# Kernel tuning notes

Hardware: AMD Instinct MI355X
Metric: run time of the kernel (lower is better)

Reference implementation:

```python
import jax, jax.numpy as jnp
import numpy as np

V, E, H, EH, IH = 32000, 512, 512, 512, 512
B, S, T = 32, 128, 64
COPY_COEFF = 1.0
BOS = 0

def setup_inputs() -> dict:
    key = jax.random.key(0)
    ks = jax.random.split(key, 12)
    n = jax.random.normal
    return {
        "trg_tokens": jax.random.randint(ks[0], (B, T), 0, V),
        "init_hidden": n(ks[1], (B, IH), jnp.float32),
        "enc_hs": n(ks[2], (S, B, EH), jnp.float32),
        "enc_idxs": jax.random.randint(ks[3], (B, S), 0, V),
        "emb": n(ks[4], (V, E), jnp.float32) * 0.02,
        "W_ih": n(ks[5], (4 * H, E), jnp.float32) * 0.04,
        "W_hh": n(ks[6], (4 * H, H), jnp.float32) * 0.04,
        "b_ih": jnp.zeros((4 * H,), jnp.float32),
        "b_hh": jnp.zeros((4 * H,), jnp.float32),
        "bridge_W": n(ks[7], (H, IH), jnp.float32) * 0.04,
        "bridge_b": jnp.zeros((H,), jnp.float32),
        "out_W": n(ks[8], (V, H), jnp.float32) * 0.04,
        "out_b": jnp.zeros((V,), jnp.float32),
        "copy_W": n(ks[9], (H, EH), jnp.float32) * 0.04,
        "copy_b": jnp.zeros((H,), jnp.float32),
    }


def _decode(trg_tokens, enc_idxs, init_hidden, enc_hs, emb, W_ih, W_hh, b_ih, b_hh,
            bridge_W, bridge_b, out_W, out_b, copy_W, copy_b):
    vocab = emb.shape[0]
    # bridge: tanh(Linear(init_hidden_size, hidden)), shared for h0 and c0
    h0 = jnp.tanh(init_hidden @ bridge_W.T + bridge_b)  # [B, H]
    c0 = h0
    # teacher-forced input tokens: [BOS, trg[0], ..., trg[T-2]]
    bos = jnp.full((trg_tokens.shape[0], 1), BOS, trg_tokens.dtype)
    tok_in = jnp.concatenate([bos, trg_tokens[:, :-1]], axis=1)  # [B, T]
    # copy features are step-invariant: tanh(copy_weights(enc_hs.transpose(0,1)))
    u_feat = jnp.tanh(jnp.einsum('sbe,he->bsh', enc_hs, copy_W) + copy_b)  # [B, S, H]

    def scatter_copy(s, idx):
        # replaces one-hot [S, V] bmm with a scatter-add: sum exp-scores per vocab id
        return jnp.zeros((vocab,), s.dtype).at[idx].add(s)

    def step(carry, tok):
        h, c = carry
        x = emb[tok]  # [B, E]
        gates = x @ W_ih.T + b_ih + h @ W_hh.T + b_hh  # [B, 4H], torch order i,f,g,o
        i, f, g, o = jnp.split(gates, 4, axis=-1)
        c = jax.nn.sigmoid(f) * c + jax.nn.sigmoid(i) * jnp.tanh(g)
        h = jax.nn.sigmoid(o) * jnp.tanh(c)
        score_gen = h @ out_W.T + out_b  # [B, V]
        u = jnp.einsum('bsh,bh->bs', u_feat, h)  # copy scores over source positions
        umax = jnp.max(u, axis=1, keepdims=True)
        ue = jnp.exp(u - umax)
        u_copy = jnp.log(jax.vmap(scatter_copy)(ue, enc_idxs) + 1e-35) + umax  # [B, V]
        scores = jax.nn.softmax(jnp.concatenate([score_gen, u_copy], axis=1), axis=1)
        proba = scores[:, :vocab] + COPY_COEFF * scores[:, vocab:]
        return (h, c), jnp.log(proba)

    (_, _), logp = jax.lax.scan(step, (h0, c0), tok_in.T)  # logp: [T, B, V]
    return logp


def reference(trg_tokens, init_hidden, enc_hs, enc_idxs, emb, W_ih, W_hh, b_ih, b_hh,
              bridge_W, bridge_b, out_W, out_b, copy_W, copy_b):
    return _decode(trg_tokens, enc_idxs, init_hidden, enc_hs, emb, W_ih, W_hh, b_ih, b_hh,
                   bridge_W, bridge_b, out_W, out_b, copy_W, copy_b)
```

## Files before the change

kernel.cpp:

```cpp
#include <hip/hip_runtime.h>
#include <stdint.h>

#define VOCAB 32000
#define HID   512
#define NBAT  32
#define NSRC  128
#define NTGT  64

typedef __attribute__((ext_vector_type(8))) __bf16 bf16x8;
typedef __attribute__((ext_vector_type(4))) float  f32x4;

__device__ __forceinline__ ushort f2bf(float f) {
  union { float f; uint32_t u; } v; v.f = f;
  uint32_t u = v.u;
  u += 0x7fffu + ((u >> 16) & 1u);
  return (ushort)(u >> 16);
}

__device__ __forceinline__ float sigmoidf_(float x) { return 1.0f / (1.0f + expf(-x)); }

__device__ __forceinline__ int swz(int row, int chunk16) {
  return (chunk16 * 16) ^ ((row & 7) * 16);
}

__device__ __forceinline__ f32x4 mfma16(bf16x8 a, bf16x8 b, f32x4 c) {
  return __builtin_amdgcn_mfma_f32_16x16x32_bf16(a, b, c, 0, 0, 0);
}

__global__ void init_kernel(const int* __restrict__ trg, int* __restrict__ tok_in,
                            const float* __restrict__ b_ih, const float* __restrict__ b_hh,
                            float* __restrict__ bsum, int* __restrict__ flags) {
  int i = blockIdx.x * 256 + threadIdx.x;
  if (i < 2048) {
    int t = i >> 5, b = i & 31;
    tok_in[i] = (t == 0) ? 0 : trg[b * NTGT + (t - 1)];
    bsum[i] = b_ih[i] + b_hh[i];
  }
  if (i < 1024) flags[i] = 0;
}

__global__ void cvt_kernel(const float* __restrict__ src, ushort* __restrict__ dst, int n4) {
  int i = blockIdx.x * 256 + threadIdx.x;
  if (i < n4) {
    float4 v = reinterpret_cast<const float4*>(src)[i];
    ushort4 o;
    o.x = f2bf(v.x); o.y = f2bf(v.y); o.z = f2bf(v.z); o.w = f2bf(v.w);
    reinterpret_cast<ushort4*>(dst)[i] = o;
  }
}

__global__ __launch_bounds__(256, 2)
void bridge_kernel(const float* __restrict__ init_hidden, const float* __restrict__ bW,
                   const float* __restrict__ bb, float* __restrict__ hbuf_f32,
                   ushort* __restrict__ hbuf_bf) {
  __shared__ float ih[512];
  int b = blockIdx.x, tid = threadIdx.x;
  ih[tid] = init_hidden[b * 512 + tid];
  ih[tid + 256] = init_hidden[b * 512 + 256 + tid];
  __syncthreads();
  for (int rep = 0; rep < 2; ++rep) {
    int j = tid + rep * 256;
    const float4* wr = reinterpret_cast<const float4*>(bW + (size_t)j * 512);
    float s = 0.0f;
    #pragma unroll 4
    for (int k = 0; k < 128; ++k) {
      float4 wv = wr[k];
      s += wv.x * ih[k*4] + wv.y * ih[k*4+1] + wv.z * ih[k*4+2] + wv.w * ih[k*4+3];
    }
    float v = tanhf(s + bb[j]);
    hbuf_f32[b * 512 + j] = v;
    hbuf_bf[b * 512 + j]  = f2bf(v);
  }
}

template<int AMODE, int TANH, int STATS>
__global__ __launch_bounds__(256, 2)
void gemm_bt(const void* __restrict__ Av, const ushort* __restrict__ Bw,
             const float* __restrict__ bias, float* __restrict__ C,
             const int* __restrict__ gidx, float2* __restrict__ partials,
             int N, int K, int PNB) {
  __shared__ __align__(16) char smem[32768];
  __shared__ float pm[128][2], ps[128][2];
  char* smA = smem;
  char* smB = smem + 16384;
  const int tid = threadIdx.x;
  const int w = tid >> 6, l = tid & 63;
  const int mb0 = blockIdx.x * 128, nb0 = blockIdx.y * 128;
  const int msub = (w & 1) * 64, nsub = (w >> 1) * 64;

  f32x4 acc[4][4] = {};
  const int kiters = K >> 6;
  for (int ki = 0; ki < kiters; ++ki) {
    __syncthreads();
    if (AMODE == 2) {
      const ushort* A16 = (const ushort*)Av;
      #pragma unroll
      for (int c = 0; c < 4; ++c) {
        int id = tid + c * 256;
        int row = id >> 3, kc = id & 7;
        uint4 av = *reinterpret_cast<const uint4*>(A16 + (size_t)(mb0 + row) * K + ki * 64 + kc * 8);
        int byte = row * 128 + swz(row, kc);
        *reinterpret_cast<uint4*>(smA + byte) = av;
      }
    } else {
      const float* A32 = (const float*)Av;
      #pragma unroll
      for (int c = 0; c < 8; ++c) {
        int id = tid + c * 256;
        int row = id >> 4, f4 = id & 15;
        int arow = (AMODE == 1) ? gidx[mb0 + row] : (mb0 + row);
        float4 av = *reinterpret_cast<const float4*>(A32 + (size_t)arow * K + ki * 64 + f4 * 4);
        uint32_t lo = (uint32_t)f2bf(av.x) | ((uint32_t)f2bf(av.y) << 16);
        uint32_t hi = (uint32_t)f2bf(av.z) | ((uint32_t)f2bf(av.w) << 16);
        int byte = row * 128 + swz(row, f4 >> 1) + (f4 & 1) * 8;
        *reinterpret_cast<uint2*>(smA + byte) = make_uint2(lo, hi);
      }
    }
    #pragma unroll
    for (int c = 0; c < 4; ++c) {
      int id = tid + c * 256;
      int row = id >> 3, kc = id & 7;
      uint4 bv = *reinterpret_cast<const uint4*>(Bw + (size_t)(nb0 + row) * K + ki * 64 + kc * 8);
      int byte = row * 128 + swz(row, kc);
      *reinterpret_cast<uint4*>(smB + byte) = bv;
    }
    __syncthreads();
    #pragma unroll
    for (int ks = 0; ks < 2; ++ks) {
      bf16x8 af[4], bfr[4];
      #pragma unroll
      for (int i = 0; i < 4; ++i) {
        int row = msub + i * 16 + (l & 15);
        af[i] = *reinterpret_cast<const bf16x8*>(smA + row * 128 + swz(row, ks * 4 + (l >> 4)));
      }
      #pragma unroll
      for (int i = 0; i < 4; ++i) {
        int row = nsub + i * 16 + (l & 15);
        bfr[i] = *reinterpret_cast<const bf16x8*>(smB + row * 128 + swz(row, ks * 4 + (l >> 4)));
      }
      #pragma unroll
      for (int mi = 0; mi < 4; ++mi)
        #pragma unroll
        for (int ni = 0; ni < 4; ++ni)
          acc[mi][ni] = mfma16(af[mi], bfr[ni], acc[mi][ni]);
    }
  }
  float bcol[4];
  #pragma unroll
  for (int ni = 0; ni < 4; ++ni)
    bcol[ni] = bias ? bias[nb0 + nsub + ni * 16 + (l & 15)] : 0.0f;
  #pragma unroll
  for (int mi = 0; mi < 4; ++mi) {
    #pragma unroll
    for (int ni = 0; ni < 4; ++ni) {
      int col = nb0 + nsub + ni * 16 + (l & 15);
      #pragma unroll
      for (int j = 0; j < 4; ++j) {
        int row = mb0 + msub + mi * 16 + (l >> 4) * 4 + j;
        float v = acc[mi][ni][j] + bcol[ni];
        acc[mi][ni][j] = v;
        if (TANH) v = tanhf(v);
        C[(size_t)row * N + col] = v;
      }
    }
  }
  if (STATS) {
    #pragma unroll
    for (int mi = 0; mi < 4; ++mi) {
      #pragma unroll
      for (int j = 0; j < 4; ++j) {
        float mx = fmaxf(fmaxf(acc[mi][0][j], acc[mi][1][j]), fmaxf(acc[mi][2][j], acc[mi][3][j]));
        #pragma unroll
        for (int d = 1; d < 16; d <<= 1) mx = fmaxf(mx, __shfl_xor(mx, d));
        float sx = expf(acc[mi][0][j] - mx) + expf(acc[mi][1][j] - mx)
                 + expf(acc[mi][2][j] - mx) + expf(acc[mi][3][j] - mx);
        #pragma unroll
        for (int d = 1; d < 16; d <<= 1) sx += __shfl_xor(sx, d);
        if ((l & 15) == 0) {
          int r = msub + mi * 16 + (l >> 4) * 4 + j;
          pm[r][w >> 1] = mx;
          ps[r][w >> 1] = sx;
        }
      }
    }
    __syncthreads();
    if (tid < 128) {
      float ma = pm[tid][0], mb = pm[tid][1];
      float m = fmaxf(ma, mb);
      float s = ps[tid][0] * expf(ma - m) + ps[tid][1] * expf(mb - m);
      partials[(size_t)(mb0 + tid) * PNB + blockIdx.y] = make_float2(m, s);
    }
  }
}

__global__ __launch_bounds__(256, 1)
void lstm_rec(const ushort* __restrict__ Whh_bf, const float* __restrict__ gates_x,
              float* __restrict__ hbuf_f32, ushort* __restrict__ hbuf_bf,
              int* __restrict__ flags) {
  __shared__ __align__(16) char h_lds[32 * 1024];
  __shared__ float gt[32 * 64];
  __shared__ float c_state[512];
  const int tid = threadIdx.x, w = tid >> 6, l = tid & 63;
  const int blk = blockIdx.x;
  const int gate0 = (w >> 1) * 2;
  const int mtile = (w & 1);

  bf16x8 wf[2][16];
  #pragma unroll
  for (int nt = 0; nt < 2; ++nt) {
    int grow = (gate0 + nt) * 512 + blk * 16 + (l & 15);
    const ushort* base = Whh_bf + (size_t)grow * 512 + (l >> 4) * 8;
    #pragma unroll
    for (int ks = 0; ks < 16; ++ks)
      wf[nt][ks] = *reinterpret_cast<const bf16x8*>(base + ks * 32);
  }

  for (int idx = tid; idx < 512; idx += 256) {
    int b = idx >> 4, cc = idx & 15;
    c_state[idx] = hbuf_f32[b * 512 + blk * 16 + cc];
  }

  float gpre[2][4];
  #pragma unroll
  for (int nt = 0; nt < 2; ++nt)
    #pragma unroll
    for (int j = 0; j < 4; ++j) {
      int b = mtile * 16 + (l >> 4) * 4 + j;
      gpre[nt][j] = gates_x[(size_t)b * 2048 + (gate0 + nt) * 512 + blk * 16 + (l & 15)];
    }

  for (int t = 0; t < NTGT; ++t) {
    const ushort* hsrc = hbuf_bf + (size_t)t * (32 * 512);
    #pragma unroll
    for (int c = 0; c < 8; ++c) {
      int id = tid + c * 256;
      int row = id >> 6, ch = id & 63;
      uint4 v = *reinterpret_cast<const uint4*>(hsrc + row * 512 + ch * 8);
      *reinterpret_cast<uint4*>(h_lds + row * 1024 + ((ch * 16) ^ ((row & 7) * 16))) = v;
    }
    __syncthreads();

    f32x4 acc[2];
    #pragma unroll
    for (int nt = 0; nt < 2; ++nt)
      #pragma unroll
      for (int j = 0; j < 4; ++j)
        acc[nt][j] = gpre[nt][j];
    #pragma unroll
    for (int ks = 0; ks < 16; ++ks) {
      int row = mtile * 16 + (l & 15);
      bf16x8 af = *reinterpret_cast<const bf16x8*>(
          h_lds + row * 1024 + (((ks * 4 + (l >> 4)) * 16) ^ ((row & 7) * 16)));
      acc[0] = mfma16(af, wf[0][ks], acc[0]);
      acc[1] = mfma16(af, wf[1][ks], acc[1]);
    }
    #pragma unroll
    for (int nt = 0; nt < 2; ++nt)
      #pragma unroll
      for (int j = 0; j < 4; ++j) {
        int b = mtile * 16 + (l >> 4) * 4 + j;
        gt[b * 64 + (gate0 + nt) * 16 + (l & 15)] = acc[nt][j];
      }
    __syncthreads();

    #pragma unroll
    for (int rep = 0; rep < 2; ++rep) {
      int idx = tid + rep * 256;
      int b = idx >> 4, cc = idx & 15;
      float gi = gt[b * 64 + cc],      gf = gt[b * 64 + 16 + cc];
      float gg = gt[b * 64 + 32 + cc], go = gt[b * 64 + 48 + cc];
      float cn = sigmoidf_(gf) * c_state[idx] + sigmoidf_(gi) * tanhf(gg);
      float hn = sigmoidf_(go) * tanhf(cn);
      c_state[idx] = cn;
      size_t o = (size_t)(t + 1) * (32 * 512) + b * 512 + blk * 16 + cc;
      hbuf_f32[o] = hn;
      __hip_atomic_store(&hbuf_bf[o], f2bf(hn), __ATOMIC_RELAXED, __HIP_MEMORY_SCOPE_AGENT);
    }
    asm volatile("s_waitcnt vmcnt(0)" ::: "memory");
    __syncthreads();
    if (tid == 0)
      __hip_atomic_store(&flags[blk * 32], t + 1, __ATOMIC_RELAXED, __HIP_MEMORY_SCOPE_AGENT);

    if (t + 1 < NTGT) {
      #pragma unroll
      for (int nt = 0; nt < 2; ++nt)
        #pragma unroll
        for (int j = 0; j < 4; ++j) {
          int b = mtile * 16 + (l >> 4) * 4 + j;
          gpre[nt][j] = gates_x[(size_t)((t + 1) * 32 + b) * 2048 + (gate0 + nt) * 512 + blk * 16 + (l & 15)];
        }
      if (w == 0) {
        int target = t + 1;
        while (true) {
          int f = (l < 32) ? __hip_atomic_load(&flags[l * 32], __ATOMIC_RELAXED, __HIP_MEMORY_SCOPE_AGENT)
                           : target;
          if (__all(f >= target)) break;
          __builtin_amdgcn_s_sleep(1);
        }
        __builtin_amdgcn_fence(__ATOMIC_ACQUIRE, "agent");
      }
      __syncthreads();
    }
  }
}

__global__ __launch_bounds__(256, 2)
void stats_kernel(const float2* __restrict__ partials, const float* __restrict__ hbuf_f32,
                  const float* __restrict__ u_feat, float* __restrict__ ue_out,
                  float4* __restrict__ stats) {
  __shared__ float red[256];
  __shared__ float hl[512];
  __shared__ float up[256];
  int r = blockIdx.x, tid = threadIdx.x;
  int t = r >> 5, b = r & 31;
  float m_i = -3.0e38f, s_i = 0.0f;
  if (tid < 250) { float2 p = partials[(size_t)r * 250 + tid]; m_i = p.x; s_i = p.y; }
  red[tid] = m_i; __syncthreads();
  for (int s = 128; s > 0; s >>= 1) { if (tid < s) red[tid] = fmaxf(red[tid], red[tid + s]); __syncthreads(); }
  float G = red[0]; __syncthreads();
  red[tid] = (tid < 250) ? s_i * expf(m_i - G) : 0.0f; __syncthreads();
  for (int s = 128; s > 0; s >>= 1) { if (tid < s) red[tid] += red[tid + s]; __syncthreads(); }
  float Sg = red[0]; __syncthreads();

  const float* hrow = hbuf_f32 + (size_t)(t + 1) * (32 * 512) + b * 512;
  hl[tid] = hrow[tid]; hl[tid + 256] = hrow[tid + 256];
  __syncthreads();
  {
    int s = tid & 127, half = tid >> 7;
    const float4* uf = reinterpret_cast<const float4*>(u_feat + (size_t)(s * 32 + b) * 512 + half * 256);
    const float* hh = hl + half * 256;
    float p = 0.0f;
    #pragma unroll 4
    for (int k = 0; k < 64; ++k) {
      float4 v = uf[k];
      p += v.x * hh[k*4] + v.y * hh[k*4+1] + v.z * hh[k*4+2] + v.w * hh[k*4+3];
    }
    up[tid] = p;
  }
  __syncthreads();
  float u = 0.0f;
  if (tid < 128) u = up[tid] + up[tid + 128];
  red[tid] = (tid < 128) ? u : -3.0e38f;
  __syncthreads();
  for (int s = 128; s > 0; s >>= 1) { if (tid < s) red[tid] = fmaxf(red[tid], red[tid + s]); __syncthreads(); }
  float umax = red[0]; __syncthreads();
  float uev = 0.0f;
  if (tid < 128) { uev = expf(u - umax); ue_out[(size_t)r * 128 + tid] = uev; }
  red[tid] = (tid < 128) ? uev : 0.0f;
  __syncthreads();
  for (int s = 128; s > 0; s >>= 1) { if (tid < s) red[tid] += red[tid + s]; __syncthreads(); }
  if (tid == 0) {
    float Sue = red[0];
    float M = fmaxf(G, umax);
    float Z = Sg * expf(G - M) + expf(umax - M) * (Sue + (float)VOCAB * 1e-35f);
    stats[r] = make_float4(M, logf(Z), expf(umax - M), 0.0f);
  }
}

__global__ __launch_bounds__(256, 4)
void transform_kernel(float* __restrict__ out, const float4* __restrict__ stats) {
  int r = blockIdx.x, tid = threadIdx.x;
  float4 st = stats[r];
  float M = st.x, logZ = st.y, c0 = st.z * 1e-35f;
  float4* row = reinterpret_cast<float4*>(out + (size_t)r * VOCAB);
  for (int i = 0; i < 32; ++i) {
    int idx = i * 256 + tid;
    if (idx < 8000) {
      float4 x = row[idx];
      x.x = logf(expf(x.x - M) + c0) - logZ;
      x.y = logf(expf(x.y - M) + c0) - logZ;
      x.z = logf(expf(x.z - M) + c0) - logZ;
      x.w = logf(expf(x.w - M) + c0) - logZ;
      row[idx] = x;
    }
  }
}

__global__ __launch_bounds__(128, 4)
void fixup_kernel(float* __restrict__ out, const float* __restrict__ hbuf_f32,
                  const float* __restrict__ ue, const int* __restrict__ enc_idxs,
                  const float* __restrict__ outW, const float* __restrict__ outb,
                  const float4* __restrict__ stats) {
  __shared__ float hl[512];
  __shared__ float uel[128];
  __shared__ int il[128];
  int r = blockIdx.x, tid = threadIdx.x;
  int t = r >> 5, b = r & 31;
  const float* hrow = hbuf_f32 + (size_t)(t + 1) * (32 * 512) + b * 512;
  for (int i = tid; i < 512; i += 128) hl[i] = hrow[i];
  uel[tid] = ue[(size_t)r * 128 + tid];
  il[tid]  = enc_idxs[b * NSRC + tid];
  __syncthreads();
  int v = il[tid];
  float scat = 0.0f;
  #pragma unroll 8
  for (int s = 0; s < 128; ++s) scat += (il[s] == v) ? uel[s] : 0.0f;
  const float4* wr = reinterpret_cast<const float4*>(outW + (size_t)v * 512);
  const float4* hf = reinterpret_cast<const float4*>(hl);
  float p = 0.0f;
  #pragma unroll 4
  for (int k = 0; k < 128; ++k) {
    float4 wv = wr[k]; float4 hv = hf[k];
    p += wv.x * hv.x + wv.y * hv.y + wv.z * hv.z + wv.w * hv.w;
  }
  p += outb[v];
  float4 st = stats[r];
  float val = logf(expf(p - st.x) + st.z * (scat + 1e-35f)) - st.y;
  out[(size_t)r * VOCAB + v] = val;
}

extern "C" void kernel_launch(void* const* d_in, const int* in_sizes, int n_in,
                              void* d_out, int out_size, void* d_ws, size_t ws_size,
                              hipStream_t stream) {
  (void)in_sizes; (void)n_in; (void)out_size; (void)ws_size;
  const int*   trg      = (const int*)  d_in[0];
  const float* init_h   = (const float*)d_in[1];
  const float* enc_hs   = (const float*)d_in[2];
  const int*   enc_idxs = (const int*)  d_in[3];
  const float* emb      = (const float*)d_in[4];
  const float* W_ih     = (const float*)d_in[5];
  const float* W_hh     = (const float*)d_in[6];
  const float* b_ih     = (const float*)d_in[7];
  const float* b_hh     = (const float*)d_in[8];
  const float* bridge_W = (const float*)d_in[9];
  const float* bridge_b = (const float*)d_in[10];
  const float* out_W    = (const float*)d_in[11];
  const float* out_b    = (const float*)d_in[12];
  const float* copy_W   = (const float*)d_in[13];
  const float* copy_b   = (const float*)d_in[14];
  float* out = (float*)d_out;

  char* ws = (char*)d_ws;
  size_t off = 0;
  auto alloc = [&](size_t bytes) -> char* {
    char* p = ws + off;
    off = (off + bytes + 255) & ~(size_t)255;
    return p;
  };
  ushort* outW_bf  = (ushort*)alloc((size_t)VOCAB * 512 * 2);
  ushort* Wih_bf   = (ushort*)alloc((size_t)2048 * 512 * 2);
  ushort* copyW_bf = (ushort*)alloc((size_t)512 * 512 * 2);
  ushort* Whh_bf   = (ushort*)alloc((size_t)2048 * 512 * 2);
  float*  u_feat   = (float*) alloc((size_t)NSRC * NBAT * 512 * 4);
  float*  gates_x  = (float*) alloc((size_t)NTGT * NBAT * 2048 * 4);
  float*  hbuf_f32 = (float*) alloc((size_t)(NTGT + 1) * NBAT * 512 * 4);
  ushort* hbuf_bf  = (ushort*)alloc((size_t)(NTGT + 1) * NBAT * 512 * 2);
  float*  ue       = (float*) alloc((size_t)2048 * 128 * 4);
  float4* stats    = (float4*)alloc((size_t)2048 * 16);
  int*    tok_in   = (int*)   alloc(2048 * 4);
  float*  bsum     = (float*) alloc(2048 * 4);
  int*    flags    = (int*)   alloc(1024 * 4);
  float2* partials = (float2*)gates_x;

  init_kernel<<<8, 256, 0, stream>>>(trg, tok_in, b_ih, b_hh, bsum, flags);
  cvt_kernel<<<(VOCAB * 512 / 4 + 255) / 256, 256, 0, stream>>>(out_W, outW_bf, VOCAB * 512 / 4);
  cvt_kernel<<<(2048 * 512 / 4 + 255) / 256, 256, 0, stream>>>(W_ih, Wih_bf, 2048 * 512 / 4);
  cvt_kernel<<<(512 * 512 / 4 + 255) / 256, 256, 0, stream>>>(copy_W, copyW_bf, 512 * 512 / 4);
  cvt_kernel<<<(2048 * 512 / 4 + 255) / 256, 256, 0, stream>>>(W_hh, Whh_bf, 2048 * 512 / 4);

  bridge_kernel<<<32, 256, 0, stream>>>(init_h, bridge_W, bridge_b, hbuf_f32, hbuf_bf);
  gemm_bt<0, 1, 0><<<dim3(32, 4), 256, 0, stream>>>(enc_hs, copyW_bf, copy_b, u_feat, nullptr, nullptr, 512, 512, 0);
  gemm_bt<1, 0, 0><<<dim3(16, 16), 256, 0, stream>>>(emb, Wih_bf, bsum, gates_x, tok_in, nullptr, 2048, 512, 0);
  lstm_rec<<<32, 256, 0, stream>>>(Whh_bf, gates_x, hbuf_f32, hbuf_bf, flags);
  gemm_bt<2, 0, 1><<<dim3(16, 250), 256, 0, stream>>>(hbuf_bf + 32 * 512, outW_bf, out_b, out, nullptr, partials, VOCAB, 512, 250);
  stats_kernel<<<2048, 256, 0, stream>>>(partials, hbuf_f32, u_feat, ue, stats);
  transform_kernel<<<2048, 256, 0, stream>>>(out, stats);
  fixup_kernel<<<2048, 128, 0, stream>>>(out, hbuf_f32, ue, enc_idxs, out_W, out_b, stats);
}
```

Baseline: 1.005 ms.

## Restructure decode pipeline: XCD-swizzled GEMMs, MFMA copy kernel, cheap transform, faster LSTM

Several changes land together. The GEMMs use a 1D grid with an XCD-aware block swizzle, and u_feat is stored as bf16. A new MFMA copy_kernel computes copy scores U and gathered generation logits P per batch, replacing per-row fp32 dot products in the stats and fixup kernels. The transform pass becomes a single subtract of M+logZ instead of log(exp()+c) per element, and the copy positions are patched afterwards by scatter_kernel. The LSTM recurrence gets fast sigmoid/tanh, float2 state, packed coherent bf16 stores and batched coherent loads of h, and drops the fp32 h buffer. Computing copy scores from bf16 h and u_feat lowers precision.

After: 893.3 us. -11.1%, faster.

```diff
diff --git a/kernel.cpp b/kernel.cpp
--- a/kernel.cpp
+++ b/kernel.cpp
@@ -17,7 +17,12 @@
   return (ushort)(u >> 16);
 }
 
-__device__ __forceinline__ float sigmoidf_(float x) { return 1.0f / (1.0f + expf(-x)); }
+__device__ __forceinline__ float fsig(float x) {
+  return __builtin_amdgcn_rcpf(1.0f + __expf(-x));
+}
+__device__ __forceinline__ float ftanh(float x) {
+  return 1.0f - 2.0f * __builtin_amdgcn_rcpf(1.0f + __expf(2.0f * x));
+}
 
 __device__ __forceinline__ int swz(int row, int chunk16) {
   return (chunk16 * 16) ^ ((row & 7) * 16);
@@ -25,6 +30,20 @@
 
 __device__ __forceinline__ f32x4 mfma16(bf16x8 a, bf16x8 b, f32x4 c) {
   return __builtin_amdgcn_mfma_f32_16x16x32_bf16(a, b, c, 0, 0, 0);
+}
+
+__device__ __forceinline__ uint4 ld_cohx4(const void* p) {
+  uint4 r;
+  asm volatile("global_load_dwordx4 %0, %1, off sc0 sc1" : "=v"(r) : "v"(p) : "memory");
+  return r;
+}
+__device__ __forceinline__ int ld_coh32(const void* p) {
+  int r;
+  asm volatile("global_load_dword %0, %1, off sc0 sc1" : "=v"(r) : "v"(p) : "memory");
+  return r;
+}
+__device__ __forceinline__ void st_coh32(void* p, uint32_t v) {
+  asm volatile("global_store_dword %0, %1, off sc0 sc1" :: "v"(p), "v"(v) : "memory");
 }
 
 __global__ void init_kernel(const int* __restrict__ trg, int* __restrict__ tok_in,
@@ -51,7 +70,7 @@
 
 __global__ __launch_bounds__(256, 2)
 void bridge_kernel(const float* __restrict__ init_hidden, const float* __restrict__ bW,
-                   const float* __restrict__ bb, float* __restrict__ hbuf_f32,
+                   const float* __restrict__ bb, float* __restrict__ h0_f32,
                    ushort* __restrict__ hbuf_bf) {
   __shared__ float ih[512];
   int b = blockIdx.x, tid = threadIdx.x;
@@ -68,15 +87,15 @@
       s += wv.x * ih[k*4] + wv.y * ih[k*4+1] + wv.z * ih[k*4+2] + wv.w * ih[k*4+3];
     }
     float v = tanhf(s + bb[j]);
-    hbuf_f32[b * 512 + j] = v;
-    hbuf_bf[b * 512 + j]  = f2bf(v);
-  }
-}
-
-template<int AMODE, int TANH, int STATS>
+    h0_f32[b * 512 + j] = v;
+    hbuf_bf[b * 512 + j] = f2bf(v);
+  }
+}
+
+template<int GX, int AMODE, int TANH, int STATS, int OUT16>
 __global__ __launch_bounds__(256, 2)
 void gemm_bt(const void* __restrict__ Av, const ushort* __restrict__ Bw,
-             const float* __restrict__ bias, float* __restrict__ C,
+             const float* __restrict__ bias, void* __restrict__ Cv,
              const int* __restrict__ gidx, float2* __restrict__ partials,
              int N, int K, int PNB) {
   __shared__ __align__(16) char smem[32768];
@@ -85,7 +104,11 @@
   char* smB = smem + 16384;
   const int tid = threadIdx.x;
   const int w = tid >> 6, l = tid & 63;
-  const int mb0 = blockIdx.x * 128, nb0 = blockIdx.y * 128;
+  const int nblk = gridDim.x;
+  const int q = nblk >> 3, rr = nblk & 7;
+  const int xcd = blockIdx.x & 7, pos = blockIdx.x >> 3;
+  const int sw = (xcd < rr ? xcd * (q + 1) : rr * (q + 1) + (xcd - rr) * q) + pos;
+  const int mb0 = (sw % GX) * 128, byc = sw / GX, nb0 = byc * 128;
   const int msub = (w & 1) * 64, nsub = (w >> 1) * 64;
 
   f32x4 acc[4][4] = {};
@@ -99,8 +122,7 @@
         int id = tid + c * 256;
         int row = id >> 3, kc = id & 7;
         uint4 av = *reinterpret_cast<const uint4*>(A16 + (size_t)(mb0 + row) * K + ki * 64 + kc * 8);
-        int byte = row * 128 + swz(row, kc);
-        *reinterpret_cast<uint4*>(smA + byte) = av;
+        *reinterpret_cast<uint4*>(smA + row * 128 + swz(row, kc)) = av;
       }
     } else {
       const float* A32 = (const float*)Av;
@@ -121,8 +143,7 @@
       int id = tid + c * 256;
       int row = id >> 3, kc = id & 7;
       uint4 bv = *reinterpret_cast<const uint4*>(Bw + (size_t)(nb0 + row) * K + ki * 64 + kc * 8);
-      int byte = row * 128 + swz(row, kc);
-      *reinterpret_cast<uint4*>(smB + byte) = bv;
+      *reinterpret_cast<uint4*>(smB + row * 128 + swz(row, kc)) = bv;
     }
     __syncthreads();
     #pragma unroll
@@ -160,7 +181,8 @@
         float v = acc[mi][ni][j] + bcol[ni];
         acc[mi][ni][j] = v;
         if (TANH) v = tanhf(v);
-        C[(size_t)row * N + col] = v;
+        if (OUT16) ((ushort*)Cv)[(size_t)row * N + col] = f2bf(v);
+        else       ((float*)Cv)[(size_t)row * N + col] = v;
       }
     }
   }
@@ -172,8 +194,8 @@
         float mx = fmaxf(fmaxf(acc[mi][0][j], acc[mi][1][j]), fmaxf(acc[mi][2][j], acc[mi][3][j]));
         #pragma unroll
         for (int d = 1; d < 16; d <<= 1) mx = fmaxf(mx, __shfl_xor(mx, d));
-        float sx = expf(acc[mi][0][j] - mx) + expf(acc[mi][1][j] - mx)
-                 + expf(acc[mi][2][j] - mx) + expf(acc[mi][3][j] - mx);
+        float sx = __expf(acc[mi][0][j] - mx) + __expf(acc[mi][1][j] - mx)
+                 + __expf(acc[mi][2][j] - mx) + __expf(acc[mi][3][j] - mx);
         #pragma unroll
         for (int d = 1; d < 16; d <<= 1) sx += __shfl_xor(sx, d);
         if ((l & 15) == 0) {
@@ -187,19 +209,19 @@
     if (tid < 128) {
       float ma = pm[tid][0], mb = pm[tid][1];
       float m = fmaxf(ma, mb);
-      float s = ps[tid][0] * expf(ma - m) + ps[tid][1] * expf(mb - m);
-      partials[(size_t)(mb0 + tid) * PNB + blockIdx.y] = make_float2(m, s);
+      float s = ps[tid][0] * __expf(ma - m) + ps[tid][1] * __expf(mb - m);
+      partials[(size_t)(mb0 + tid) * PNB + byc] = make_float2(m, s);
     }
   }
 }
 
 __global__ __launch_bounds__(256, 1)
 void lstm_rec(const ushort* __restrict__ Whh_bf, const float* __restrict__ gates_x,
-              float* __restrict__ hbuf_f32, ushort* __restrict__ hbuf_bf,
+              const float* __restrict__ h0_f32, ushort* __restrict__ hbuf_bf,
               int* __restrict__ flags) {
   __shared__ __align__(16) char h_lds[32 * 1024];
   __shared__ float gt[32 * 64];
-  __shared__ float c_state[512];
+  __shared__ float2 c_state[256];
   const int tid = threadIdx.x, w = tid >> 6, l = tid & 63;
   const int blk = blockIdx.x;
   const int gate0 = (w >> 1) * 2;
@@ -215,9 +237,9 @@
       wf[nt][ks] = *reinterpret_cast<const bf16x8*>(base + ks * 32);
   }
 
-  for (int idx = tid; idx < 512; idx += 256) {
-    int b = idx >> 4, cc = idx & 15;
-    c_state[idx] = hbuf_f32[b * 512 + blk * 16 + cc];
+  {
+    int b = tid >> 3, c2 = (tid & 7) * 2;
+    c_state[tid] = *reinterpret_cast<const float2*>(h0_f32 + b * 512 + blk * 16 + c2);
   }
 
   float gpre[2][4];
@@ -231,12 +253,19 @@
 
   for (int t = 0; t < NTGT; ++t) {
     const ushort* hsrc = hbuf_bf + (size_t)t * (32 * 512);
+    uint4 hv[8];
+    #pragma unroll
+    for (int c = 0; c < 8; ++c) {
+      int id = tid + c * 256;
+      hv[c] = ld_cohx4(hsrc + (id >> 6) * 512 + (id & 63) * 8);
+    }
+    asm volatile("s_waitcnt vmcnt(0)" ::: "memory");
+    __builtin_amdgcn_sched_barrier(0);
     #pragma unroll
     for (int c = 0; c < 8; ++c) {
       int id = tid + c * 256;
       int row = id >> 6, ch = id & 63;
-      uint4 v = *reinterpret_cast<const uint4*>(hsrc + row * 512 + ch * 8);
-      *reinterpret_cast<uint4*>(h_lds + row * 1024 + ((ch * 16) ^ ((row & 7) * 16))) = v;
+      *reinterpret_cast<uint4*>(h_lds + row * 1024 + ((ch * 16) ^ ((row & 7) * 16))) = hv[c];
     }
     __syncthreads();
 
@@ -263,23 +292,25 @@
       }
     __syncthreads();
 
-    #pragma unroll
-    for (int rep = 0; rep < 2; ++rep) {
-      int idx = tid + rep * 256;
-      int b = idx >> 4, cc = idx & 15;
-      float gi = gt[b * 64 + cc],      gf = gt[b * 64 + 16 + cc];
-      float gg = gt[b * 64 + 32 + cc], go = gt[b * 64 + 48 + cc];
-      float cn = sigmoidf_(gf) * c_state[idx] + sigmoidf_(gi) * tanhf(gg);
-      float hn = sigmoidf_(go) * tanhf(cn);
-      c_state[idx] = cn;
-      size_t o = (size_t)(t + 1) * (32 * 512) + b * 512 + blk * 16 + cc;
-      hbuf_f32[o] = hn;
-      __hip_atomic_store(&hbuf_bf[o], f2bf(hn), __ATOMIC_RELAXED, __HIP_MEMORY_SCOPE_AGENT);
+    {
+      int b = tid >> 3, c2 = (tid & 7) * 2;
+      const float2* g2 = reinterpret_cast<const float2*>(gt);
+      float2 gi = g2[(b * 64 +  0 + c2) >> 1];
+      float2 gf = g2[(b * 64 + 16 + c2) >> 1];
+      float2 gg = g2[(b * 64 + 32 + c2) >> 1];
+      float2 go = g2[(b * 64 + 48 + c2) >> 1];
+      float2 cs = c_state[tid];
+      float cn0 = fsig(gf.x) * cs.x + fsig(gi.x) * ftanh(gg.x);
+      float cn1 = fsig(gf.y) * cs.y + fsig(gi.y) * ftanh(gg.y);
+      float hn0 = fsig(go.x) * ftanh(cn0);
+      float hn1 = fsig(go.y) * ftanh(cn1);
+      c_state[tid] = make_float2(cn0, cn1);
+      uint32_t pk = (uint32_t)f2bf(hn0) | ((uint32_t)f2bf(hn1) << 16);
+      st_coh32(hbuf_bf + (size_t)(t + 1) * (32 * 512) + b * 512 + blk * 16 + c2, pk);
     }
     asm volatile("s_waitcnt vmcnt(0)" ::: "memory");
     __syncthreads();
-    if (tid == 0)
-      __hip_atomic_store(&flags[blk * 32], t + 1, __ATOMIC_RELAXED, __HIP_MEMORY_SCOPE_AGENT);
+    if (tid == 0) st_coh32(flags + blk * 32, (uint32_t)(t + 1));
 
     if (t + 1 < NTGT) {
       #pragma unroll
@@ -291,13 +322,13 @@
         }
       if (w == 0) {
         int target = t + 1;
+        const int* fp = flags + (l & 31) * 32;
         while (true) {
-          int f = (l < 32) ? __hip_atomic_load(&flags[l * 32], __ATOMIC_RELAXED, __HIP_MEMORY_SCOPE_AGENT)
-                           : target;
+          int f = ld_coh32(fp);
+          asm volatile("s_waitcnt vmcnt(0)" ::: "memory");
           if (__all(f >= target)) break;
           __builtin_amdgcn_s_sleep(1);
         }
-        __builtin_amdgcn_fence(__ATOMIC_ACQUIRE, "agent");
       }
       __syncthreads();
     }
@@ -305,55 +336,67 @@
 }
 
 __global__ __launch_bounds__(256, 2)
-void stats_kernel(const float2* __restrict__ partials, const float* __restrict__ hbuf_f32,
-                  const float* __restrict__ u_feat, float* __restrict__ ue_out,
+void copy_kernel(const ushort* __restrict__ hbuf_bf, const ushort* __restrict__ u_feat_bf,
+                 const ushort* __restrict__ outW_bf, const float* __restrict__ out_b,
+                 const int* __restrict__ enc_idxs, float* __restrict__ U, float* __restrict__ P) {
+  __shared__ int il[128];
+  __shared__ float ob[128];
+  int b = blockIdx.x, tid = threadIdx.x, w = tid >> 6, l = tid & 63;
+  if (tid < 128) { int v = enc_idxs[b * 128 + tid]; il[tid] = v; ob[tid] = out_b[v]; }
+  __syncthreads();
+  f32x4 aU[8] = {}, aP[8] = {};
+  const int t_lane = w * 16 + (l & 15);
+  const ushort* arow = hbuf_bf + ((size_t)(t_lane + 1) * 32 + b) * 512 + (l >> 4) * 8;
+  for (int ks = 0; ks < 16; ++ks) {
+    bf16x8 af = *reinterpret_cast<const bf16x8*>(arow + ks * 32);
+    #pragma unroll
+    for (int ni = 0; ni < 8; ++ni) {
+      int s = ni * 16 + (l & 15);
+      bf16x8 bu = *reinterpret_cast<const bf16x8*>(u_feat_bf + ((size_t)s * 32 + b) * 512 + ks * 32 + (l >> 4) * 8);
+      aU[ni] = mfma16(af, bu, aU[ni]);
+      bf16x8 bp = *reinterpret_cast<const bf16x8*>(outW_bf + (size_t)il[s] * 512 + ks * 32 + (l >> 4) * 8);
+      aP[ni] = mfma16(af, bp, aP[ni]);
+    }
+  }
+  #pragma unroll
+  for (int ni = 0; ni < 8; ++ni) {
+    int s = ni * 16 + (l & 15);
+    #pragma unroll
+    for (int j = 0; j < 4; ++j) {
+      int t = w * 16 + (l >> 4) * 4 + j;
+      size_t r = (size_t)(t * 32 + b) * 128 + s;
+      U[r] = aU[ni][j];
+      P[r] = aP[ni][j] + ob[s];
+    }
+  }
+}
+
+__global__ __launch_bounds__(256, 2)
+void stats_kernel(const float2* __restrict__ partials, const float* __restrict__ U,
                   float4* __restrict__ stats) {
   __shared__ float red[256];
-  __shared__ float hl[512];
-  __shared__ float up[256];
   int r = blockIdx.x, tid = threadIdx.x;
-  int t = r >> 5, b = r & 31;
   float m_i = -3.0e38f, s_i = 0.0f;
   if (tid < 250) { float2 p = partials[(size_t)r * 250 + tid]; m_i = p.x; s_i = p.y; }
   red[tid] = m_i; __syncthreads();
   for (int s = 128; s > 0; s >>= 1) { if (tid < s) red[tid] = fmaxf(red[tid], red[tid + s]); __syncthreads(); }
   float G = red[0]; __syncthreads();
-  red[tid] = (tid < 250) ? s_i * expf(m_i - G) : 0.0f; __syncthreads();
+  red[tid] = (tid < 250) ? s_i * __expf(m_i - G) : 0.0f; __syncthreads();
   for (int s = 128; s > 0; s >>= 1) { if (tid < s) red[tid] += red[tid + s]; __syncthreads(); }
   float Sg = red[0]; __syncthreads();
 
-  const float* hrow = hbuf_f32 + (size_t)(t + 1) * (32 * 512) + b * 512;
-  hl[tid] = hrow[tid]; hl[tid + 256] = hrow[tid + 256];
-  __syncthreads();
-  {
-    int s = tid & 127, half = tid >> 7;
-    const float4* uf = reinterpret_cast<const float4*>(u_feat + (size_t)(s * 32 + b) * 512 + half * 256);
-    const float* hh = hl + half * 256;
-    float p = 0.0f;
-    #pragma unroll 4
-    for (int k = 0; k < 64; ++k) {
-      float4 v = uf[k];
-      p += v.x * hh[k*4] + v.y * hh[k*4+1] + v.z * hh[k*4+2] + v.w * hh[k*4+3];
-    }
-    up[tid] = p;
-  }
-  __syncthreads();
-  float u = 0.0f;
-  if (tid < 128) u = up[tid] + up[tid + 128];
-  red[tid] = (tid < 128) ? u : -3.0e38f;
-  __syncthreads();
+  float u = (tid < 128) ? U[(size_t)r * 128 + tid] : -3.0e38f;
+  red[tid] = u; __syncthreads();
   for (int s = 128; s > 0; s >>= 1) { if (tid < s) red[tid] = fmaxf(red[tid], red[tid + s]); __syncthreads(); }
   float umax = red[0]; __syncthreads();
-  float uev = 0.0f;
-  if (tid < 128) { uev = expf(u - umax); ue_out[(size_t)r * 128 + tid] = uev; }
-  red[tid] = (tid < 128) ? uev : 0.0f;
-  __syncthreads();
+  red[tid] = (tid < 128) ? __expf(u - umax) : 0.0f; __syncthreads();
   for (int s = 128; s > 0; s >>= 1) { if (tid < s) red[tid] += red[tid + s]; __syncthreads(); }
   if (tid == 0) {
     float Sue = red[0];
     float M = fmaxf(G, umax);
-    float Z = Sg * expf(G - M) + expf(umax - M) * (Sue + (float)VOCAB * 1e-35f);
-    stats[r] = make_float4(M, logf(Z), expf(umax - M), 0.0f);
+    float eum = __expf(umax - M);
+    float Z = Sg * __expf(G - M) + eum * (Sue + (float)VOCAB * 1e-35f);
+    stats[r] = make_float4(M, logf(Z), eum, umax);
   }
 }
 
@@ -361,51 +404,36 @@
 void transform_kernel(float* __restrict__ out, const float4* __restrict__ stats) {
   int r = blockIdx.x, tid = threadIdx.x;
   float4 st = stats[r];
-  float M = st.x, logZ = st.y, c0 = st.z * 1e-35f;
+  float sh = st.x + st.y;
   float4* row = reinterpret_cast<float4*>(out + (size_t)r * VOCAB);
   for (int i = 0; i < 32; ++i) {
     int idx = i * 256 + tid;
     if (idx < 8000) {
       float4 x = row[idx];
-      x.x = logf(expf(x.x - M) + c0) - logZ;
-      x.y = logf(expf(x.y - M) + c0) - logZ;
-      x.z = logf(expf(x.z - M) + c0) - logZ;
-      x.w = logf(expf(x.w - M) + c0) - logZ;
+      x.x -= sh; x.y -= sh; x.z -= sh; x.w -= sh;
       row[idx] = x;
     }
   }
 }
 
 __global__ __launch_bounds__(128, 4)
-void fixup_kernel(float* __restrict__ out, const float* __restrict__ hbuf_f32,
-                  const float* __restrict__ ue, const int* __restrict__ enc_idxs,
-                  const float* __restrict__ outW, const float* __restrict__ outb,
-                  const float4* __restrict__ stats) {
-  __shared__ float hl[512];
+void scatter_kernel(float* __restrict__ out, const float* __restrict__ U,
+                    const float* __restrict__ P, const int* __restrict__ enc_idxs,
+                    const float4* __restrict__ stats) {
   __shared__ float uel[128];
   __shared__ int il[128];
-  int r = blockIdx.x, tid = threadIdx.x;
-  int t = r >> 5, b = r & 31;
-  const float* hrow = hbuf_f32 + (size_t)(t + 1) * (32 * 512) + b * 512;
-  for (int i = tid; i < 512; i += 128) hl[i] = hrow[i];
-  uel[tid] = ue[(size_t)r * 128 + tid];
-  il[tid]  = enc_idxs[b * NSRC + tid];
+  int r = blockIdx.x, tid = threadIdx.x, b = r & 31;
+  float4 st = stats[r];
+  float M = st.x, logZ = st.y, eum = st.z, umax = st.w;
+  int v = enc_idxs[b * NSRC + tid]; il[tid] = v;
+  float uev = __expf(U[(size_t)r * 128 + tid] - umax);
+  uel[tid] = uev;
   __syncthreads();
-  int v = il[tid];
   float scat = 0.0f;
   #pragma unroll 8
   for (int s = 0; s < 128; ++s) scat += (il[s] == v) ? uel[s] : 0.0f;
-  const float4* wr = reinterpret_cast<const float4*>(outW + (size_t)v * 512);
-  const float4* hf = reinterpret_cast<const float4*>(hl);
-  float p = 0.0f;
-  #pragma unroll 4
-  for (int k = 0; k < 128; ++k) {
-    float4 wv = wr[k]; float4 hv = hf[k];
-    p += wv.x * hv.x + wv.y * hv.y + wv.z * hv.z + wv.w * hv.w;
-  }
-  p += outb[v];
-  float4 st = stats[r];
-  float val = logf(expf(p - st.x) + st.z * (scat + 1e-35f)) - st.y;
+  float p = P[(size_t)r * 128 + tid];
+  float val = logf(expf(p - M) + eum * (scat + 1e-35f)) - logZ;
   out[(size_t)r * VOCAB + v] = val;
 }
 
@@ -441,11 +469,12 @@
   ushort* Wih_bf   = (ushort*)alloc((size_t)2048 * 512 * 2);
   ushort* copyW_bf = (ushort*)alloc((size_t)512 * 512 * 2);
   ushort* Whh_bf   = (ushort*)alloc((size_t)2048 * 512 * 2);
-  float*  u_feat   = (float*) alloc((size_t)NSRC * NBAT * 512 * 4);
+  ushort* u_feat_bf= (ushort*)alloc((size_t)NSRC * NBAT * 512 * 2);
   float*  gates_x  = (float*) alloc((size_t)NTGT * NBAT * 2048 * 4);
-  float*  hbuf_f32 = (float*) alloc((size_t)(NTGT + 1) * NBAT * 512 * 4);
+  float*  h0_f32   = (float*) alloc((size_t)NBAT * 512 * 4);
   ushort* hbuf_bf  = (ushort*)alloc((size_t)(NTGT + 1) * NBAT * 512 * 2);
-  float*  ue       = (float*) alloc((size_t)2048 * 128 * 4);
+  float*  U        = (float*) alloc((size_t)2048 * 128 * 4);
+  float*  P        = (float*) alloc((size_t)2048 * 128 * 4);
   float4* stats    = (float4*)alloc((size_t)2048 * 16);
   int*    tok_in   = (int*)   alloc(2048 * 4);
   float*  bsum     = (float*) alloc(2048 * 4);
@@ -458,12 +487,13 @@
   cvt_kernel<<<(512 * 512 / 4 + 255) / 256, 256, 0, stream>>>(copy_W, copyW_bf, 512 * 512 / 4);
   cvt_kernel<<<(2048 * 512 / 4 + 255) / 256, 256, 0, stream>>>(W_hh, Whh_bf, 2048 * 512 / 4);
 
-  bridge_kernel<<<32, 256, 0, stream>>>(init_h, bridge_W, bridge_b, hbuf_f32, hbuf_bf);
-  gemm_bt<0, 1, 0><<<dim3(32, 4), 256, 0, stream>>>(enc_hs, copyW_bf, copy_b, u_feat, nullptr, nullptr, 512, 512, 0);
-  gemm_bt<1, 0, 0><<<dim3(16, 16), 256, 0, stream>>>(emb, Wih_bf, bsum, gates_x, tok_in, nullptr, 2048, 512, 0);
-  lstm_rec<<<32, 256, 0, stream>>>(Whh_bf, gates_x, hbuf_f32, hbuf_bf, flags);
-  gemm_bt<2, 0, 1><<<dim3(16, 250), 256, 0, stream>>>(hbuf_bf + 32 * 512, outW_bf, out_b, out, nullptr, partials, VOCAB, 512, 250);
-  stats_kernel<<<2048, 256, 0, stream>>>(partials, hbuf_f32, u_feat, ue, stats);
+  bridge_kernel<<<32, 256, 0, stream>>>(init_h, bridge_W, bridge_b, h0_f32, hbuf_bf);
+  gemm_bt<32, 0, 1, 0, 1><<<128, 256, 0, stream>>>(enc_hs, copyW_bf, copy_b, u_feat_bf, nullptr, nullptr, 512, 512, 0);
+  gemm_bt<16, 1, 0, 0, 0><<<256, 256, 0, stream>>>(emb, Wih_bf, bsum, gates_x, tok_in, nullptr, 2048, 512, 0);
+  lstm_rec<<<32, 256, 0, stream>>>(Whh_bf, gates_x, h0_f32, hbuf_bf, flags);
+  gemm_bt<16, 2, 0, 1, 0><<<4000, 256, 0, stream>>>(hbuf_bf + 32 * 512, outW_bf, out_b, out, nullptr, partials, VOCAB, 512, 250);
+  copy_kernel<<<32, 256, 0, stream>>>(hbuf_bf, u_feat_bf, outW_bf, out_b, enc_idxs, U, P);
+  stats_kernel<<<2048, 256, 0, stream>>>(partials, U, stats);
   transform_kernel<<<2048, 256, 0, stream>>>(out, stats);
-  fixup_kernel<<<2048, 128, 0, stream>>>(out, hbuf_f32, ue, enc_idxs, out_W, out_b, stats);
-}
+  scatter_kernel<<<2048, 128, 0, stream>>>(out, U, P, enc_idxs, stats);
+}
```
